# Kernel optimization log

Measured on AMD Instinct MI355X. Metric: run time of the kernel, lower is better.

Reference implementation:

```python
import jax, jax.numpy as jnp
import numpy as np

SQRT_2_OVER_PI = 0.7978845608028654

def gelu_tanh(x):
    return 0.5 * x * (1.0 + jnp.tanh(SQRT_2_OVER_PI * (x + 0.044715 * x ** 3)))

def setup_inputs() -> dict:
    key = jax.random.key(0)
    ks = jax.random.split(key, 16)
    B, L, H, Dk, Dv = 4, 512, 8, 64, 64
    dm = H * Dk
    inp = {
        'q': jax.random.normal(ks[0], (B, L, dm), jnp.float32),
        'k': jax.random.normal(ks[1], (B, L, dm), jnp.float32),
        'v': jax.random.normal(ks[2], (B, L, dm), jnp.float32),
        'vec_adj_k': jax.random.normal(ks[3], (B, L, L, Dk), jnp.float32),
        'vec_adj_v': jax.random.normal(ks[4], (B, L, L, Dv), jnp.float32),
        'adj_k': jax.random.randint(ks[5], (B, L, L), 0, 2, jnp.int32),
        'adj_v': jax.random.randint(ks[6], (B, L, L), 0, 2, jnp.int32),
        # learned params (Linear weights stored as [in, out]; y = x @ W)
        'w_qs': jax.random.normal(ks[7], (dm, H * Dk), jnp.float32) * 0.02,
        'w_ks': jax.random.normal(ks[8], (dm, H * Dk), jnp.float32) * 0.02,
        'w_vs': jax.random.normal(ks[9], (dm, H * Dv), jnp.float32) * 0.02,
        'w_fc': jax.random.normal(ks[10], (H * Dk, H * Dk), jnp.float32) * 0.02,
        'w_nw': jax.random.normal(ks[11], (H * Dk, 1), jnp.float32) * 0.02,
        'w_self': jax.random.normal(ks[12], (H * Dk, H * Dk), jnp.float32) * 0.02,
        'w_dd': jax.random.normal(ks[13], (H * Dk, H * Dk), jnp.float32) * 0.02,
    }
    return inp

def reference(q, k, v, vec_adj_k, vec_adj_v, adj_k, adj_v,
              w_qs, w_ks, w_vs, w_fc, w_nw, w_self, w_dd):
    H, Dk, Dv = 8, 64, 64
    B, L, dm = q.shape
    temperature = Dk ** 0.5
    residual = q
    # projections -> [B, H, L, D]
    qh = (q @ w_qs).reshape(B, L, H, Dk).transpose(0, 2, 1, 3)
    kh = (k @ w_ks).reshape(B, L, H, Dk).transpose(0, 2, 1, 3)
    vh = (v @ w_vs).reshape(B, L, H, Dv).transpose(0, 2, 1, 3)
    qs = qh / temperature
    # inner_(q, k, vec_adj_k, flag=True): content + relative-position scores
    scores = jnp.einsum('bhld,bhmd->bhlm', qs, kh) \
           + jnp.einsum('bhld,blmd->bhlm', qs, vec_adj_k)  # [B,H,L,L]
    # adjacency mask (mask == 0 -> -10000)
    scores = jnp.where(adj_k[:, None, :, :] == 0, jnp.float32(-10000.0), scores)
    attn = jax.nn.softmax(scores, axis=-1)
    # inner_(attn, v, vec_adj_v, flag=False)
    out = jnp.einsum('bhlm,bhmd->bhld', attn, vh) \
        + jnp.einsum('bhlm,blmd->bhld', attn, vec_adj_v)
    qc = out.transpose(0, 2, 1, 3).reshape(B, L, H * Dv)  # [B,L,dm]
    # masked neighbor aggregation (GNN stage)
    adj_f = adj_k.astype(qc.dtype)
    nn_num = adj_f.sum(-1)                                  # [B,L]
    denom = jnp.where(nn_num >= 1.0, nn_num, 1.0)
    node_weight = jax.nn.sigmoid((qc @ w_nw)[..., 0])       # [B,L]
    self_info = qc @ w_self
    dd_info = qc @ w_dd
    dd_weight = node_weight[:, None, :] * adj_f             # [B,L,L]
    agg = jnp.matmul(dd_weight, dd_info) / denom[..., None]
    qo = gelu_tanh((self_info + agg) @ w_fc)
    qo = residual + qo
    return (qo, attn)
```

## Files before the change

kernel.cpp:

```cpp
#include <hip/hip_runtime.h>
#include <cstdint>

#define NB 4
#define NL 512
#define NH 8
#define ND 64
#define NDM 512

typedef __attribute__((ext_vector_type(8))) short short8;
typedef __attribute__((ext_vector_type(4))) float f32x4;

__device__ __forceinline__ unsigned short f2bf(float f){
  union { float f; unsigned u; } v; v.f = f;
  unsigned r = (v.u + 0x7fffu + ((v.u >> 16) & 1u)) >> 16;
  return (unsigned short)r;
}

__device__ __forceinline__ short8 ld8(const unsigned short* p){
  return *(const short8*)p;
}

__device__ __forceinline__ f32x4 mfma16(short8 a, short8 b, f32x4 c){
  return __builtin_amdgcn_mfma_f32_16x16x32_bf16(a, b, c, 0, 0, 0);
}

__device__ __forceinline__ float gelu_tanh(float x){
  float u = 0.7978845608028654f * (x + 0.044715f * x * x * x);
  return 0.5f * x * (1.f + tanhf(u));
}

__global__ __launch_bounds__(256) void k_prep(const float* __restrict__ q,
    const float* __restrict__ k, const float* __restrict__ v,
    unsigned short* __restrict__ xin,
    const float* __restrict__ wqs, const float* __restrict__ wks,
    const float* __restrict__ wvs, const float* __restrict__ wself,
    const float* __restrict__ wdd, const float* __restrict__ wfc,
    unsigned short* __restrict__ Wt){
  int blk = blockIdx.x;
  int t = threadIdx.x;
  if (blk < 3072){
    int i = blk * 256 + t;
    int w = i >> 18, r = i & 262143;
    const float* src = (w == 0) ? q : (w == 1) ? k : v;
    float4 f = *(const float4*)(src + (size_t)r * 4);
    unsigned lo = (unsigned)f2bf(f.x) | ((unsigned)f2bf(f.y) << 16);
    unsigned hi = (unsigned)f2bf(f.z) | ((unsigned)f2bf(f.w) << 16);
    uint2 o; o.x = lo; o.y = hi;
    *(uint2*)(xin + (size_t)w * 1048576 + (size_t)r * 4) = o;
  } else {
    int i = (blk - 3072) * 256 + t;
    int w = i >> 13;
    int rr = i & 8191;
    int kg = rr >> 9;
    int n  = rr & 511;
    int k0 = kg * 32;
    const float* src = (w == 0) ? wqs : (w == 1) ? wks : (w == 2) ? wvs :
                       (w == 3) ? wself : (w == 4) ? wdd : wfc;
    unsigned pk[16];
#pragma unroll
    for (int j = 0; j < 16; j++){
      float a = src[(size_t)(k0 + 2 * j) * 512 + n];
      float b = src[(size_t)(k0 + 2 * j + 1) * 512 + n];
      pk[j] = (unsigned)f2bf(a) | ((unsigned)f2bf(b) << 16);
    }
    uint4* o4 = (uint4*)(Wt + (size_t)w * 262144 + (size_t)n * 512 + k0);
    o4[0] = make_uint4(pk[0],  pk[1],  pk[2],  pk[3]);
    o4[1] = make_uint4(pk[4],  pk[5],  pk[6],  pk[7]);
    o4[2] = make_uint4(pk[8],  pk[9],  pk[10], pk[11]);
    o4[3] = make_uint4(pk[12], pk[13], pk[14], pk[15]);
  }
}

__global__ __launch_bounds__(256) void k_proj(const unsigned short* __restrict__ xin,
    const unsigned short* __restrict__ Wt, unsigned short* __restrict__ qsb,
    unsigned short* __restrict__ khb, unsigned short* __restrict__ vhT){
  int wid0 = blockIdx.x * 4 + (threadIdx.x >> 6);
  int mode = wid0 >> 10;
  int wid = wid0 & 1023;
  int lane = threadIdx.x & 63;
  int tm = wid >> 5, tn = wid & 31;
  int r = lane & 15, q = lane >> 4;
  const unsigned short* X = xin + (size_t)mode * 1048576;
  const unsigned short* W = Wt + (size_t)mode * 262144;
  unsigned short* dst = (mode == 0) ? qsb : (mode == 1) ? khb : vhT;
  const unsigned short* A  = X + (size_t)(tm * 16 + r) * 512 + q * 8;
  const unsigned short* Bp = W + (size_t)(tn * 16 + r) * 512 + q * 8;
  f32x4 acc = {0.f, 0.f, 0.f, 0.f};
  for (int kk = 0; kk < 512; kk += 32) acc = mfma16(ld8(A + kk), ld8(Bp + kk), acc);
  int col = tn * 16 + r;
  int h = col >> 6, d = col & 63;
  float sc = (mode == 0) ? 0.125f : 1.0f;
  for (int i = 0; i < 4; i++){
    int row = tm * 16 + q * 4 + i;
    int b = row >> 9, l = row & 511;
    float vv = acc[i] * sc;
    size_t idx = (mode == 2) ? ((size_t)((b * 8 + h) * 64 + d) * 512 + l)
                             : ((size_t)((b * 8 + h) * 512 + l) * 64 + d);
    dst[idx] = f2bf(vv);
  }
}

__global__ __launch_bounds__(256) void k_scores(const unsigned short* __restrict__ qs,
    const unsigned short* __restrict__ kh, float* __restrict__ attnF){
  int wid = blockIdx.x * 4 + (threadIdx.x >> 6);
  int lane = threadIdx.x & 63;
  int bh = wid >> 8;
  int rest = wid & 255;
  int tm = rest >> 3, tg = rest & 7;
  int r = lane & 15, q = lane >> 4;
  const unsigned short* A = qs + (size_t)bh * 512 * 64 + (size_t)(tm * 16 + r) * 64 + q * 8;
  short8 a0 = ld8(A), a1 = ld8(A + 32);
  float* C = attnF + (size_t)bh * 512 * 512;
  for (int tn = tg * 4; tn < tg * 4 + 4; tn++){
    const unsigned short* Bp = kh + (size_t)bh * 512 * 64 + (size_t)(tn * 16 + r) * 64 + q * 8;
    f32x4 acc = {0.f, 0.f, 0.f, 0.f};
    acc = mfma16(a0, ld8(Bp),      acc);
    acc = mfma16(a1, ld8(Bp + 32), acc);
    for (int i = 0; i < 4; i++){
      int row = tm * 16 + q * 4 + i;
      C[(size_t)row * 512 + tn * 16 + r] = acc[i];
    }
  }
}

__global__ __launch_bounds__(256) void k_relsoft(const unsigned short* __restrict__ qs,
    const float* __restrict__ vak, const int* __restrict__ adj,
    float* __restrict__ attnF, unsigned short* __restrict__ attn_bf){
  int bid = blockIdx.x;
  int b = bid >> 9, l = bid & 511;
  int t = threadIdx.x, lane = t & 63, w = t >> 6;
  __shared__ __align__(16) unsigned short qsA[16 * 64];
  __shared__ __align__(16) unsigned short vkt[128 * 72];
  __shared__ float sc[8 * 512];
  __shared__ int adjs[512];
  for (int j = 0; j < 4; j++){
    int e = t + j * 256;
    int m = e >> 6, d = e & 63;
    qsA[e] = (m < 8) ? qs[((size_t)((b * 8 + m) * 512 + l)) * 64 + d] : (unsigned short)0;
  }
  for (int j = 0; j < 16; j++){
    int e = t + j * 256;
    int h = e >> 9, m = e & 511;
    sc[e] = attnF[((size_t)(b * 8 + h) * 512 + l) * 512 + m];
  }
  adjs[t]       = adj[(size_t)bid * 512 + t];
  adjs[t + 256] = adj[(size_t)bid * 512 + t + 256];
  __syncthreads();
  int r = lane & 15, q = lane >> 4;
  short8 a0 = ld8(qsA + r * 64 + q * 8);
  short8 a1 = ld8(qsA + r * 64 + 32 + q * 8);
  const float* vrow = vak + (size_t)bid * 512 * 64;
  for (int c = 0; c < 4; c++){
    for (int it = 0; it < 8; it++){
      int i4 = it * 256 + t;
      int m = i4 >> 4, d4 = (i4 & 15) * 4;
      const float4 f = *(const float4*)(vrow + (size_t)(c * 128 + m) * 64 + d4);
      unsigned p0 = (unsigned)f2bf(f.x) | ((unsigned)f2bf(f.y) << 16);
      unsigned p1 = (unsigned)f2bf(f.z) | ((unsigned)f2bf(f.w) << 16);
      uint2 pp; pp.x = p0; pp.y = p1;
      *(uint2*)(&vkt[m * 72 + d4]) = pp;
    }
    __syncthreads();
    for (int nt2 = 0; nt2 < 2; nt2++){
      int nt = w * 2 + nt2;
      const unsigned short* bp = vkt + (nt * 16 + r) * 72 + q * 8;
      f32x4 acc = {0.f, 0.f, 0.f, 0.f};
      acc = mfma16(a0, ld8(bp),      acc);
      acc = mfma16(a1, ld8(bp + 32), acc);
      if (q < 2){
        for (int i = 0; i < 4; i++){
          int h = q * 4 + i;
          sc[h * 512 + c * 128 + nt * 16 + r] += acc[i];
        }
      }
    }
    __syncthreads();
  }
  for (int hh = 0; hh < 2; hh++){
    int h = w * 2 + hh;
    float v[8]; float mx = -3.0e38f;
    for (int i = 0; i < 8; i++){
      int m = lane + i * 64;
      float s = sc[h * 512 + m];
      if (adjs[m] == 0) s = -10000.0f;
      v[i] = s; mx = fmaxf(mx, s);
    }
    for (int off = 32; off; off >>= 1) mx = fmaxf(mx, __shfl_xor(mx, off, 64));
    float sum = 0.f;
    for (int i = 0; i < 8; i++){ v[i] = __expf(v[i] - mx); sum += v[i]; }
    for (int off = 32; off; off >>= 1) sum += __shfl_xor(sum, off, 64);
    float inv = 1.f / sum;
    size_t base = ((size_t)(b * 8 + h) * 512 + l) * 512;
    for (int i = 0; i < 8; i++){
      int m = lane + i * 64;
      float p2 = v[i] * inv;
      attnF[base + m] = p2;
      attn_bf[base + m] = f2bf(p2);
    }
  }
}

__global__ __launch_bounds__(256) void k_outc(const unsigned short* __restrict__ attn_bf,
    const unsigned short* __restrict__ vhT, float* __restrict__ qc){
  int wid = blockIdx.x * 4 + (threadIdx.x >> 6);
  int lane = threadIdx.x & 63;
  int bh = wid >> 7, tile = wid & 127;
  int tm = tile >> 2, tn = tile & 3;
  int r = lane & 15, q = lane >> 4;
  const unsigned short* A  = attn_bf + (size_t)bh * 512 * 512 + (size_t)(tm * 16 + r) * 512 + q * 8;
  const unsigned short* Bp = vhT + (size_t)bh * 64 * 512 + (size_t)(tn * 16 + r) * 512 + q * 8;
  f32x4 acc = {0.f, 0.f, 0.f, 0.f};
  for (int k = 0; k < 512; k += 32) acc = mfma16(ld8(A + k), ld8(Bp + k), acc);
  int b = bh >> 3, h = bh & 7;
  int d = tn * 16 + r;
  for (int i = 0; i < 4; i++){
    int lrow = tm * 16 + q * 4 + i;
    qc[(size_t)(b * 512 + lrow) * 512 + h * 64 + d] = acc[i];
  }
}

__global__ __launch_bounds__(256) void k_outrel(const unsigned short* __restrict__ attn_bf,
    const float* __restrict__ vav, const float* __restrict__ qc,
    const int* __restrict__ adj, const float* __restrict__ wnw,
    unsigned short* __restrict__ qc_bf, float* __restrict__ nw, float* __restrict__ invden){
  int bid = blockIdx.x;
  int b = bid >> 9, l = bid & 511;
  int t = threadIdx.x, lane = t & 63, w = t >> 6;
  __shared__ __align__(16) unsigned short vvT[64 * 136];
  __shared__ float orL[512];
  __shared__ float redf[4];
  __shared__ int redi[4];
  int r = lane & 15, q = lane >> 4;
  int h8 = r & 7;
  const float* vrow = vav + (size_t)bid * 512 * 64;
  const unsigned short* arow = attn_bf + ((size_t)(b * 8 + h8) * 512 + l) * 512;
  f32x4 acc = {0.f, 0.f, 0.f, 0.f};
  for (int c = 0; c < 4; c++){
    for (int it = 0; it < 8; it++){
      int i4 = it * 256 + t;
      int m = i4 >> 4, d4 = (i4 & 15) * 4;
      const float4 f = *(const float4*)(vrow + (size_t)(c * 128 + m) * 64 + d4);
      vvT[(d4    ) * 136 + m] = f2bf(f.x);
      vvT[(d4 + 1) * 136 + m] = f2bf(f.y);
      vvT[(d4 + 2) * 136 + m] = f2bf(f.z);
      vvT[(d4 + 3) * 136 + m] = f2bf(f.w);
    }
    __syncthreads();
    for (int s = 0; s < 4; s++){
      int kk = c * 128 + s * 32;
      short8 av = ld8(arow + kk + q * 8);
      short8 bv = ld8(vvT + (w * 16 + r) * 136 + s * 32 + q * 8);
      acc = mfma16(av, bv, acc);
    }
    __syncthreads();
  }
  if (q < 2){
    for (int i = 0; i < 4; i++){
      int h = q * 4 + i;
      orL[h * 64 + w * 16 + r] = acc[i];
    }
  }
  __syncthreads();
  float part = 0.f; int asum = 0;
  for (int j = 0; j < 2; j++){
    int e = t + j * 256;
    float val = qc[(size_t)bid * 512 + e] + orL[e];
    qc_bf[(size_t)bid * 512 + e] = f2bf(val);
    part += val * wnw[e];
    asum += adj[(size_t)bid * 512 + e];
  }
  for (int off = 32; off; off >>= 1){
    part += __shfl_xor(part, off, 64);
    asum += __shfl_xor(asum, off, 64);
  }
  if (lane == 0){ redf[w] = part; redi[w] = asum; }
  __syncthreads();
  if (t == 0){
    float tot = redf[0] + redf[1] + redf[2] + redf[3];
    int at = redi[0] + redi[1] + redi[2] + redi[3];
    nw[bid] = 1.f / (1.f + __expf(-tot));
    invden[bid] = 1.f / ((at >= 1) ? (float)at : 1.f);
  }
}

__global__ __launch_bounds__(256) void k_post(const unsigned short* __restrict__ qcb,
    const unsigned short* __restrict__ Wself, const unsigned short* __restrict__ Wdd,
    float* __restrict__ selfi, unsigned short* __restrict__ ddT,
    const int* __restrict__ adj, const float* __restrict__ nw,
    const float* __restrict__ invden, unsigned short* __restrict__ ddw){
  __shared__ __align__(16) unsigned short ldsT[64 * 20];
  int blk = blockIdx.x;
  int t = threadIdx.x;
  if (blk < 2048){
    int mode = blk >> 10;
    int wv = t >> 6;
    int wid = (blk & 1023) * 4 + wv;
    int lane = t & 63;
    int tm = wid >> 5, tn = wid & 31;
    int r = lane & 15, q = lane >> 4;
    const unsigned short* W = mode ? Wdd : Wself;
    const unsigned short* A  = qcb + (size_t)(tm * 16 + r) * 512 + q * 8;
    const unsigned short* Bp = W + (size_t)(tn * 16 + r) * 512 + q * 8;
    f32x4 acc = {0.f, 0.f, 0.f, 0.f};
    for (int kk = 0; kk < 512; kk += 32) acc = mfma16(ld8(A + kk), ld8(Bp + kk), acc);
    int col = tn * 16 + r;
    if (mode == 0){
      for (int i = 0; i < 4; i++){
        int row = tm * 16 + q * 4 + i;
        selfi[(size_t)row * 512 + col] = acc[i];
      }
    } else {
      int nLocal = wv * 16 + r;
      for (int i = 0; i < 4; i++) ldsT[nLocal * 20 + q * 4 + i] = f2bf(acc[i]);
      __syncthreads();
      int tmB = ((blk & 1023) * 4) >> 5;
      int tnBase = ((blk & 1023) * 4) & 31;
      int n = t >> 2, part = t & 3;
      ushort4 val = *(const ushort4*)(&ldsT[n * 20 + part * 4]);
      int b = (tmB * 16) >> 9;
      int m0 = (tmB * 16) & 511;
      int nGlob = tnBase * 16 + n;
      *(ushort4*)(&ddT[((size_t)(b * 512 + nGlob)) * 512 + m0 + part * 4]) = val;
    }
  } else {
    int i = (blk - 2048) * 256 + t;
    int b = i >> 18, rest = i & 262143;
    int l = rest >> 9, m = rest & 511;
    int a = adj[i];
    float v = a ? nw[b * 512 + m] * invden[b * 512 + l] : 0.f;
    ddw[i] = f2bf(v);
  }
}

__global__ __launch_bounds__(256) void k_agg(const unsigned short* __restrict__ ddw,
    const unsigned short* __restrict__ ddT, const float* __restrict__ selfi,
    unsigned short* __restrict__ xbf){
  int wid = blockIdx.x * 4 + (threadIdx.x >> 6);
  int lane = threadIdx.x & 63;
  int b = wid >> 10, tile = wid & 1023;
  int tm = tile >> 5, tn = tile & 31;
  int r = lane & 15, q = lane >> 4;
  const unsigned short* A  = ddw + (size_t)b * 262144 + (size_t)(tm * 16 + r) * 512 + q * 8;
  const unsigned short* Bp = ddT + (size_t)b * 262144 + (size_t)(tn * 16 + r) * 512 + q * 8;
  f32x4 acc = {0.f, 0.f, 0.f, 0.f};
  for (int k = 0; k < 512; k += 32) acc = mfma16(ld8(A + k), ld8(Bp + k), acc);
  int col = tn * 16 + r;
  for (int i = 0; i < 4; i++){
    int row = b * 512 + tm * 16 + q * 4 + i;
    float x = acc[i] + selfi[(size_t)row * 512 + col];
    xbf[(size_t)row * 512 + col] = f2bf(x);
  }
}

__global__ __launch_bounds__(256) void k_fc(const unsigned short* __restrict__ xbf,
    const unsigned short* __restrict__ W, const float* __restrict__ qin,
    float* __restrict__ qo){
  int wid = blockIdx.x * 4 + (threadIdx.x >> 6);
  int lane = threadIdx.x & 63;
  int tm = wid >> 5, tn = wid & 31;
  int r = lane & 15, q = lane >> 4;
  const unsigned short* A  = xbf + (size_t)(tm * 16 + r) * 512 + q * 8;
  const unsigned short* Bp = W + (size_t)(tn * 16 + r) * 512 + q * 8;
  f32x4 acc = {0.f, 0.f, 0.f, 0.f};
  for (int k = 0; k < 512; k += 32) acc = mfma16(ld8(A + k), ld8(Bp + k), acc);
  int col = tn * 16 + r;
  for (int i = 0; i < 4; i++){
    int row = tm * 16 + q * 4 + i;
    qo[(size_t)row * 512 + col] = qin[(size_t)row * 512 + col] + gelu_tanh(acc[i]);
  }
}

extern "C" void kernel_launch(void* const* d_in, const int* in_sizes, int n_in,
                              void* d_out, int out_size, void* d_ws, size_t ws_size,
                              hipStream_t stream){
  const float* q    = (const float*)d_in[0];
  const float* k    = (const float*)d_in[1];
  const float* v    = (const float*)d_in[2];
  const float* vak  = (const float*)d_in[3];
  const float* vav  = (const float*)d_in[4];
  const int*   adjk = (const int*)d_in[5];
  const float* wqs  = (const float*)d_in[7];
  const float* wks  = (const float*)d_in[8];
  const float* wvs  = (const float*)d_in[9];
  const float* wfc  = (const float*)d_in[10];
  const float* wnw  = (const float*)d_in[11];
  const float* wself= (const float*)d_in[12];
  const float* wdd  = (const float*)d_in[13];

  float* qo    = (float*)d_out;
  float* attnF = qo + 1048576;

  char* p = (char*)d_ws;
  unsigned short* xin   = (unsigned short*)p; p += 6291456;
  unsigned short* Wt    = (unsigned short*)p; p += 3145728;
  unsigned short* qsb   = (unsigned short*)p; p += 2097152;
  unsigned short* khb   = (unsigned short*)p; p += 2097152;
  unsigned short* vhT   = (unsigned short*)p; p += 2097152;
  unsigned short* attnb = (unsigned short*)p; p += 16777216;
  float*          qc    = (float*)p;          p += 4194304;
  unsigned short* qcb   = (unsigned short*)p; p += 2097152;
  float*          nw    = (float*)p;          p += 8192;
  float*          invd  = (float*)p;          p += 8192;
  float*          selfi = (float*)p;          p += 4194304;
  unsigned short* ddT   = (unsigned short*)p; p += 2097152;
  unsigned short* ddw   = (unsigned short*)p; p += 2097152;
  unsigned short* xbf   = (unsigned short*)p; p += 2097152;

  k_prep<<<3264, 256, 0, stream>>>(q, k, v, xin, wqs, wks, wvs, wself, wdd, wfc, Wt);
  k_proj<<<3072, 256, 0, stream>>>(xin, Wt, qsb, khb, vhT);
  k_scores<<<2048, 256, 0, stream>>>(qsb, khb, attnF);
  k_relsoft<<<2048, 256, 0, stream>>>(qsb, vak, adjk, attnF, attnb);
  k_outc<<<1024, 256, 0, stream>>>(attnb, vhT, qc);
  k_outrel<<<2048, 256, 0, stream>>>(attnb, vav, qc, adjk, wnw, qcb, nw, invd);
  k_post<<<6144, 256, 0, stream>>>(qcb, Wt + 786432, Wt + 1048576, selfi, ddT,
                                   adjk, nw, invd, ddw);
  k_agg<<<1024, 256, 0, stream>>>(ddw, ddT, selfi, xbf);
  k_fc<<<1024, 256, 0, stream>>>(xbf, Wt + 1310720, q, qo);
}
```

Before: 713.7 us.

## Use 64x64 per-wave MFMA tiles and drop LDS staging in relative kernels

```diff
diff --git a/kernel.cpp b/kernel.cpp
--- a/kernel.cpp
+++ b/kernel.cpp
@@ -1,11 +1,6 @@
 #include <hip/hip_runtime.h>
 #include <cstdint>
 
-#define NB 4
-#define NL 512
-#define NH 8
-#define ND 64
-#define NDM 512
 
 typedef __attribute__((ext_vector_type(8))) short short8;
 typedef __attribute__((ext_vector_type(4))) float f32x4;
@@ -27,6 +22,36 @@
 __device__ __forceinline__ float gelu_tanh(float x){
   float u = 0.7978845608028654f * (x + 0.044715f * x * x * x);
   return 0.5f * x * (1.f + tanhf(u));
+}
+
+__device__ __forceinline__ short8 pack8(float4 f0, float4 f1){
+  short8 s;
+  s[0] = (short)f2bf(f0.x); s[1] = (short)f2bf(f0.y);
+  s[2] = (short)f2bf(f0.z); s[3] = (short)f2bf(f0.w);
+  s[4] = (short)f2bf(f1.x); s[5] = (short)f2bf(f1.y);
+  s[6] = (short)f2bf(f1.z); s[7] = (short)f2bf(f1.w);
+  return s;
+}
+
+template<int LDA, int LDB, int KSTEPS>
+__device__ __forceinline__ void gemm64(const unsigned short* __restrict__ A,
+                                       const unsigned short* __restrict__ Bp,
+                                       f32x4 acc[4][4]){
+#pragma unroll 2
+  for (int ks = 0; ks < KSTEPS; ks++){
+    int kk = ks * 32;
+    short8 a[4], b[4];
+#pragma unroll
+    for (int i = 0; i < 4; i++){
+      a[i] = ld8(A + (size_t)i * 16 * LDA + kk);
+      b[i] = ld8(Bp + (size_t)i * 16 * LDB + kk);
+    }
+#pragma unroll
+    for (int i = 0; i < 4; i++)
+#pragma unroll
+      for (int j = 0; j < 4; j++)
+        acc[i][j] = mfma16(a[i], b[j], acc[i][j]);
+  }
 }
 
 __global__ __launch_bounds__(256) void k_prep(const float* __restrict__ q,
@@ -74,53 +99,60 @@
 __global__ __launch_bounds__(256) void k_proj(const unsigned short* __restrict__ xin,
     const unsigned short* __restrict__ Wt, unsigned short* __restrict__ qsb,
     unsigned short* __restrict__ khb, unsigned short* __restrict__ vhT){
-  int wid0 = blockIdx.x * 4 + (threadIdx.x >> 6);
-  int mode = wid0 >> 10;
-  int wid = wid0 & 1023;
+  int wid = blockIdx.x * 4 + (threadIdx.x >> 6);
+  int mode = wid >> 8;
+  int tile = wid & 255;
+  int tm = tile >> 3, tn = tile & 7;
   int lane = threadIdx.x & 63;
-  int tm = wid >> 5, tn = wid & 31;
-  int r = lane & 15, q = lane >> 4;
+  int r = lane & 15, qq = lane >> 4;
   const unsigned short* X = xin + (size_t)mode * 1048576;
   const unsigned short* W = Wt + (size_t)mode * 262144;
   unsigned short* dst = (mode == 0) ? qsb : (mode == 1) ? khb : vhT;
-  const unsigned short* A  = X + (size_t)(tm * 16 + r) * 512 + q * 8;
-  const unsigned short* Bp = W + (size_t)(tn * 16 + r) * 512 + q * 8;
-  f32x4 acc = {0.f, 0.f, 0.f, 0.f};
-  for (int kk = 0; kk < 512; kk += 32) acc = mfma16(ld8(A + kk), ld8(Bp + kk), acc);
-  int col = tn * 16 + r;
-  int h = col >> 6, d = col & 63;
-  float sc = (mode == 0) ? 0.125f : 1.0f;
-  for (int i = 0; i < 4; i++){
-    int row = tm * 16 + q * 4 + i;
-    int b = row >> 9, l = row & 511;
-    float vv = acc[i] * sc;
-    size_t idx = (mode == 2) ? ((size_t)((b * 8 + h) * 64 + d) * 512 + l)
-                             : ((size_t)((b * 8 + h) * 512 + l) * 64 + d);
-    dst[idx] = f2bf(vv);
-  }
+  const unsigned short* A  = X + (size_t)(tm * 64 + r) * 512 + qq * 8;
+  const unsigned short* Bp = W + (size_t)(tn * 64 + r) * 512 + qq * 8;
+  f32x4 acc[4][4] = {};
+  gemm64<512, 512, 16>(A, Bp, acc);
+  float scv = (mode == 0) ? 0.125f : 1.0f;
+  int h = tn;
+#pragma unroll
+  for (int i = 0; i < 4; i++)
+#pragma unroll
+    for (int j = 0; j < 4; j++)
+#pragma unroll
+      for (int e = 0; e < 4; e++){
+        int row = tm * 64 + i * 16 + qq * 4 + e;
+        int d = j * 16 + r;
+        int bb = row >> 9, l = row & 511;
+        unsigned short val = f2bf(acc[i][j][e] * scv);
+        size_t idx = (mode == 2) ? ((size_t)((bb * 8 + h) * 64 + d) * 512 + l)
+                                 : ((size_t)((bb * 8 + h) * 512 + l) * 64 + d);
+        dst[idx] = val;
+      }
 }
 
 __global__ __launch_bounds__(256) void k_scores(const unsigned short* __restrict__ qs,
     const unsigned short* __restrict__ kh, float* __restrict__ attnF){
   int wid = blockIdx.x * 4 + (threadIdx.x >> 6);
+  int bh = wid >> 6;
+  int tile = wid & 63;
+  int tm = tile >> 3, tn = tile & 7;
   int lane = threadIdx.x & 63;
-  int bh = wid >> 8;
-  int rest = wid & 255;
-  int tm = rest >> 3, tg = rest & 7;
-  int r = lane & 15, q = lane >> 4;
-  const unsigned short* A = qs + (size_t)bh * 512 * 64 + (size_t)(tm * 16 + r) * 64 + q * 8;
-  short8 a0 = ld8(A), a1 = ld8(A + 32);
-  float* C = attnF + (size_t)bh * 512 * 512;
-  for (int tn = tg * 4; tn < tg * 4 + 4; tn++){
-    const unsigned short* Bp = kh + (size_t)bh * 512 * 64 + (size_t)(tn * 16 + r) * 64 + q * 8;
-    f32x4 acc = {0.f, 0.f, 0.f, 0.f};
-    acc = mfma16(a0, ld8(Bp),      acc);
-    acc = mfma16(a1, ld8(Bp + 32), acc);
-    for (int i = 0; i < 4; i++){
-      int row = tm * 16 + q * 4 + i;
-      C[(size_t)row * 512 + tn * 16 + r] = acc[i];
-    }
-  }
+  int r = lane & 15, qq = lane >> 4;
+  const unsigned short* A  = qs + (size_t)bh * 32768 + (size_t)(tm * 64 + r) * 64 + qq * 8;
+  const unsigned short* Bp = kh + (size_t)bh * 32768 + (size_t)(tn * 64 + r) * 64 + qq * 8;
+  f32x4 acc[4][4] = {};
+  gemm64<64, 64, 2>(A, Bp, acc);
+  float* C = attnF + (size_t)bh * 262144;
+#pragma unroll
+  for (int i = 0; i < 4; i++)
+#pragma unroll
+    for (int j = 0; j < 4; j++)
+#pragma unroll
+      for (int e = 0; e < 4; e++){
+        int row = tm * 64 + i * 16 + qq * 4 + e;
+        int col = tn * 64 + j * 16 + r;
+        C[(size_t)row * 512 + col] = acc[i][j][e];
+      }
 }
 
 __global__ __launch_bounds__(256) void k_relsoft(const unsigned short* __restrict__ qs,
@@ -130,7 +162,6 @@
   int b = bid >> 9, l = bid & 511;
   int t = threadIdx.x, lane = t & 63, w = t >> 6;
   __shared__ __align__(16) unsigned short qsA[16 * 64];
-  __shared__ __align__(16) unsigned short vkt[128 * 72];
   __shared__ float sc[8 * 512];
   __shared__ int adjs[512];
   for (int j = 0; j < 4; j++){
@@ -146,36 +177,34 @@
   adjs[t]       = adj[(size_t)bid * 512 + t];
   adjs[t + 256] = adj[(size_t)bid * 512 + t + 256];
   __syncthreads();
-  int r = lane & 15, q = lane >> 4;
-  short8 a0 = ld8(qsA + r * 64 + q * 8);
-  short8 a1 = ld8(qsA + r * 64 + 32 + q * 8);
-  const float* vrow = vak + (size_t)bid * 512 * 64;
+  int r = lane & 15, qq = lane >> 4;
+  short8 a0 = ld8(qsA + r * 64 + qq * 8);
+  short8 a1 = ld8(qsA + r * 64 + 32 + qq * 8);
+  const float* vrow = vak + (size_t)bid * 32768;
+#pragma unroll
   for (int c = 0; c < 4; c++){
-    for (int it = 0; it < 8; it++){
-      int i4 = it * 256 + t;
-      int m = i4 >> 4, d4 = (i4 & 15) * 4;
-      const float4 f = *(const float4*)(vrow + (size_t)(c * 128 + m) * 64 + d4);
-      unsigned p0 = (unsigned)f2bf(f.x) | ((unsigned)f2bf(f.y) << 16);
-      unsigned p1 = (unsigned)f2bf(f.z) | ((unsigned)f2bf(f.w) << 16);
-      uint2 pp; pp.x = p0; pp.y = p1;
-      *(uint2*)(&vkt[m * 72 + d4]) = pp;
-    }
-    __syncthreads();
+#pragma unroll
     for (int nt2 = 0; nt2 < 2; nt2++){
       int nt = w * 2 + nt2;
-      const unsigned short* bp = vkt + (nt * 16 + r) * 72 + q * 8;
+      int m0 = c * 128 + nt * 16 + r;
+      const float* p = vrow + (size_t)m0 * 64 + qq * 8;
+      float4 f0 = *(const float4*)(p);
+      float4 f1 = *(const float4*)(p + 4);
+      float4 f2 = *(const float4*)(p + 32);
+      float4 f3 = *(const float4*)(p + 36);
       f32x4 acc = {0.f, 0.f, 0.f, 0.f};
-      acc = mfma16(a0, ld8(bp),      acc);
-      acc = mfma16(a1, ld8(bp + 32), acc);
-      if (q < 2){
+      acc = mfma16(a0, pack8(f0, f1), acc);
+      acc = mfma16(a1, pack8(f2, f3), acc);
+      if (qq < 2){
+#pragma unroll
         for (int i = 0; i < 4; i++){
-          int h = q * 4 + i;
+          int h = qq * 4 + i;
           sc[h * 512 + c * 128 + nt * 16 + r] += acc[i];
         }
       }
     }
-    __syncthreads();
-  }
+  }
+  __syncthreads();
   for (int hh = 0; hh < 2; hh++){
     int h = w * 2 + hh;
     float v[8]; float mx = -3.0e38f;
@@ -203,20 +232,25 @@
 __global__ __launch_bounds__(256) void k_outc(const unsigned short* __restrict__ attn_bf,
     const unsigned short* __restrict__ vhT, float* __restrict__ qc){
   int wid = blockIdx.x * 4 + (threadIdx.x >> 6);
+  int bh = wid >> 3;
+  int tm = wid & 7;
   int lane = threadIdx.x & 63;
-  int bh = wid >> 7, tile = wid & 127;
-  int tm = tile >> 2, tn = tile & 3;
-  int r = lane & 15, q = lane >> 4;
-  const unsigned short* A  = attn_bf + (size_t)bh * 512 * 512 + (size_t)(tm * 16 + r) * 512 + q * 8;
-  const unsigned short* Bp = vhT + (size_t)bh * 64 * 512 + (size_t)(tn * 16 + r) * 512 + q * 8;
-  f32x4 acc = {0.f, 0.f, 0.f, 0.f};
-  for (int k = 0; k < 512; k += 32) acc = mfma16(ld8(A + k), ld8(Bp + k), acc);
+  int r = lane & 15, qq = lane >> 4;
+  const unsigned short* A  = attn_bf + (size_t)bh * 262144 + (size_t)(tm * 64 + r) * 512 + qq * 8;
+  const unsigned short* Bp = vhT + (size_t)bh * 32768 + (size_t)r * 512 + qq * 8;
+  f32x4 acc[4][4] = {};
+  gemm64<512, 512, 16>(A, Bp, acc);
   int b = bh >> 3, h = bh & 7;
-  int d = tn * 16 + r;
-  for (int i = 0; i < 4; i++){
-    int lrow = tm * 16 + q * 4 + i;
-    qc[(size_t)(b * 512 + lrow) * 512 + h * 64 + d] = acc[i];
-  }
+#pragma unroll
+  for (int i = 0; i < 4; i++)
+#pragma unroll
+    for (int j = 0; j < 4; j++)
+#pragma unroll
+      for (int e = 0; e < 4; e++){
+        int lrow = tm * 64 + i * 16 + qq * 4 + e;
+        int d = j * 16 + r;
+        qc[(size_t)(b * 512 + lrow) * 512 + h * 64 + d] = acc[i][j][e];
+      }
 }
 
 __global__ __launch_bounds__(256) void k_outrel(const unsigned short* __restrict__ attn_bf,
@@ -226,38 +260,36 @@
   int bid = blockIdx.x;
   int b = bid >> 9, l = bid & 511;
   int t = threadIdx.x, lane = t & 63, w = t >> 6;
-  __shared__ __align__(16) unsigned short vvT[64 * 136];
   __shared__ float orL[512];
   __shared__ float redf[4];
   __shared__ int redi[4];
-  int r = lane & 15, q = lane >> 4;
+  int r = lane & 15, qq = lane >> 4;
   int h8 = r & 7;
-  const float* vrow = vav + (size_t)bid * 512 * 64;
+  const float* vrow = vav + (size_t)bid * 32768;
   const unsigned short* arow = attn_bf + ((size_t)(b * 8 + h8) * 512 + l) * 512;
   f32x4 acc = {0.f, 0.f, 0.f, 0.f};
+  int dcol = w * 16 + r;
+#pragma unroll
   for (int c = 0; c < 4; c++){
-    for (int it = 0; it < 8; it++){
-      int i4 = it * 256 + t;
-      int m = i4 >> 4, d4 = (i4 & 15) * 4;
-      const float4 f = *(const float4*)(vrow + (size_t)(c * 128 + m) * 64 + d4);
-      vvT[(d4    ) * 136 + m] = f2bf(f.x);
-      vvT[(d4 + 1) * 136 + m] = f2bf(f.y);
-      vvT[(d4 + 2) * 136 + m] = f2bf(f.z);
-      vvT[(d4 + 3) * 136 + m] = f2bf(f.w);
-    }
-    __syncthreads();
+#pragma unroll
     for (int s = 0; s < 4; s++){
       int kk = c * 128 + s * 32;
-      short8 av = ld8(arow + kk + q * 8);
-      short8 bv = ld8(vvT + (w * 16 + r) * 136 + s * 32 + q * 8);
+      short8 av = ld8(arow + kk + qq * 8);
+      float fv[8];
+#pragma unroll
+      for (int j = 0; j < 8; j++)
+        fv[j] = vrow[(size_t)(kk + qq * 8 + j) * 64 + dcol];
+      short8 bv;
+#pragma unroll
+      for (int j = 0; j < 8; j++) bv[j] = (short)f2bf(fv[j]);
       acc = mfma16(av, bv, acc);
     }
-    __syncthreads();
-  }
-  if (q < 2){
+  }
+  if (qq < 2){
+#pragma unroll
     for (int i = 0; i < 4; i++){
-      int h = q * 4 + i;
-      orL[h * 64 + w * 16 + r] = acc[i];
+      int h = qq * 4 + i;
+      orL[h * 64 + dcol] = acc[i];
     }
   }
   __syncthreads();
@@ -288,47 +320,52 @@
     float* __restrict__ selfi, unsigned short* __restrict__ ddT,
     const int* __restrict__ adj, const float* __restrict__ nw,
     const float* __restrict__ invden, unsigned short* __restrict__ ddw){
-  __shared__ __align__(16) unsigned short ldsT[64 * 20];
   int blk = blockIdx.x;
   int t = threadIdx.x;
-  if (blk < 2048){
-    int mode = blk >> 10;
-    int wv = t >> 6;
-    int wid = (blk & 1023) * 4 + wv;
+  if (blk < 128){
+    int mode = blk >> 6;
+    int wid = (blk & 63) * 4 + (t >> 6);
+    int tm = wid >> 3, tn = wid & 7;
     int lane = t & 63;
-    int tm = wid >> 5, tn = wid & 31;
-    int r = lane & 15, q = lane >> 4;
+    int r = lane & 15, qq = lane >> 4;
     const unsigned short* W = mode ? Wdd : Wself;
-    const unsigned short* A  = qcb + (size_t)(tm * 16 + r) * 512 + q * 8;
-    const unsigned short* Bp = W + (size_t)(tn * 16 + r) * 512 + q * 8;
-    f32x4 acc = {0.f, 0.f, 0.f, 0.f};
-    for (int kk = 0; kk < 512; kk += 32) acc = mfma16(ld8(A + kk), ld8(Bp + kk), acc);
-    int col = tn * 16 + r;
-    if (mode == 0){
-      for (int i = 0; i < 4; i++){
-        int row = tm * 16 + q * 4 + i;
-        selfi[(size_t)row * 512 + col] = acc[i];
-      }
-    } else {
-      int nLocal = wv * 16 + r;
-      for (int i = 0; i < 4; i++) ldsT[nLocal * 20 + q * 4 + i] = f2bf(acc[i]);
-      __syncthreads();
-      int tmB = ((blk & 1023) * 4) >> 5;
-      int tnBase = ((blk & 1023) * 4) & 31;
-      int n = t >> 2, part = t & 3;
-      ushort4 val = *(const ushort4*)(&ldsT[n * 20 + part * 4]);
-      int b = (tmB * 16) >> 9;
-      int m0 = (tmB * 16) & 511;
-      int nGlob = tnBase * 16 + n;
-      *(ushort4*)(&ddT[((size_t)(b * 512 + nGlob)) * 512 + m0 + part * 4]) = val;
-    }
+    const unsigned short* A  = qcb + (size_t)(tm * 64 + r) * 512 + qq * 8;
+    const unsigned short* Bp = W + (size_t)(tn * 64 + r) * 512 + qq * 8;
+    f32x4 acc[4][4] = {};
+    gemm64<512, 512, 16>(A, Bp, acc);
+#pragma unroll
+    for (int i = 0; i < 4; i++)
+#pragma unroll
+      for (int j = 0; j < 4; j++)
+#pragma unroll
+        for (int e = 0; e < 4; e++){
+          int row = tm * 64 + i * 16 + qq * 4 + e;
+          int col = tn * 64 + j * 16 + r;
+          if (mode == 0)
+            selfi[(size_t)row * 512 + col] = acc[i][j][e];
+          else {
+            int bb = row >> 9, m = row & 511;
+            ddT[((size_t)(bb * 512 + col)) * 512 + m] = f2bf(acc[i][j][e]);
+          }
+        }
   } else {
-    int i = (blk - 2048) * 256 + t;
-    int b = i >> 18, rest = i & 262143;
-    int l = rest >> 9, m = rest & 511;
-    int a = adj[i];
-    float v = a ? nw[b * 512 + m] * invden[b * 512 + l] : 0.f;
-    ddw[i] = f2bf(v);
+    int i8 = ((blk - 128) * 256 + t) * 8;
+    int bb = i8 >> 18, rest = i8 & 262143;
+    int l = rest >> 9, m0 = rest & 511;
+    int4 a0 = *(const int4*)(adj + i8);
+    int4 a1 = *(const int4*)(adj + i8 + 4);
+    float id = invden[bb * 512 + l];
+    const float* nwb = nw + bb * 512 + m0;
+    short8 o;
+    o[0] = a0.x ? (short)f2bf(nwb[0] * id) : (short)0;
+    o[1] = a0.y ? (short)f2bf(nwb[1] * id) : (short)0;
+    o[2] = a0.z ? (short)f2bf(nwb[2] * id) : (short)0;
+    o[3] = a0.w ? (short)f2bf(nwb[3] * id) : (short)0;
+    o[4] = a1.x ? (short)f2bf(nwb[4] * id) : (short)0;
+    o[5] = a1.y ? (short)f2bf(nwb[5] * id) : (short)0;
+    o[6] = a1.z ? (short)f2bf(nwb[6] * id) : (short)0;
+    o[7] = a1.w ? (short)f2bf(nwb[7] * id) : (short)0;
+    *(short8*)(ddw + i8) = o;
   }
 }
 
@@ -336,38 +373,49 @@
     const unsigned short* __restrict__ ddT, const float* __restrict__ selfi,
     unsigned short* __restrict__ xbf){
   int wid = blockIdx.x * 4 + (threadIdx.x >> 6);
+  int b = wid >> 6;
+  int tile = wid & 63;
+  int tm = tile >> 3, tn = tile & 7;
   int lane = threadIdx.x & 63;
-  int b = wid >> 10, tile = wid & 1023;
-  int tm = tile >> 5, tn = tile & 31;
-  int r = lane & 15, q = lane >> 4;
-  const unsigned short* A  = ddw + (size_t)b * 262144 + (size_t)(tm * 16 + r) * 512 + q * 8;
-  const unsigned short* Bp = ddT + (size_t)b * 262144 + (size_t)(tn * 16 + r) * 512 + q * 8;
-  f32x4 acc = {0.f, 0.f, 0.f, 0.f};
-  for (int k = 0; k < 512; k += 32) acc = mfma16(ld8(A + k), ld8(Bp + k), acc);
-  int col = tn * 16 + r;
-  for (int i = 0; i < 4; i++){
-    int row = b * 512 + tm * 16 + q * 4 + i;
-    float x = acc[i] + selfi[(size_t)row * 512 + col];
-    xbf[(size_t)row * 512 + col] = f2bf(x);
-  }
+  int r = lane & 15, qq = lane >> 4;
+  const unsigned short* A  = ddw + (size_t)b * 262144 + (size_t)(tm * 64 + r) * 512 + qq * 8;
+  const unsigned short* Bp = ddT + (size_t)b * 262144 + (size_t)(tn * 64 + r) * 512 + qq * 8;
+  f32x4 acc[4][4] = {};
+  gemm64<512, 512, 16>(A, Bp, acc);
+#pragma unroll
+  for (int i = 0; i < 4; i++)
+#pragma unroll
+    for (int j = 0; j < 4; j++)
+#pragma unroll
+      for (int e = 0; e < 4; e++){
+        int row = b * 512 + tm * 64 + i * 16 + qq * 4 + e;
+        int col = tn * 64 + j * 16 + r;
+        float x = acc[i][j][e] + selfi[(size_t)row * 512 + col];
+        xbf[(size_t)row * 512 + col] = f2bf(x);
+      }
 }
 
 __global__ __launch_bounds__(256) void k_fc(const unsigned short* __restrict__ xbf,
     const unsigned short* __restrict__ W, const float* __restrict__ qin,
     float* __restrict__ qo){
   int wid = blockIdx.x * 4 + (threadIdx.x >> 6);
+  int tm = wid >> 3, tn = wid & 7;
   int lane = threadIdx.x & 63;
-  int tm = wid >> 5, tn = wid & 31;
-  int r = lane & 15, q = lane >> 4;
-  const unsigned short* A  = xbf + (size_t)(tm * 16 + r) * 512 + q * 8;
-  const unsigned short* Bp = W + (size_t)(tn * 16 + r) * 512 + q * 8;
-  f32x4 acc = {0.f, 0.f, 0.f, 0.f};
-  for (int k = 0; k < 512; k += 32) acc = mfma16(ld8(A + k), ld8(Bp + k), acc);
-  int col = tn * 16 + r;
-  for (int i = 0; i < 4; i++){
-    int row = tm * 16 + q * 4 + i;
-    qo[(size_t)row * 512 + col] = qin[(size_t)row * 512 + col] + gelu_tanh(acc[i]);
-  }
+  int r = lane & 15, qq = lane >> 4;
+  const unsigned short* A  = xbf + (size_t)(tm * 64 + r) * 512 + qq * 8;
+  const unsigned short* Bp = W + (size_t)(tn * 64 + r) * 512 + qq * 8;
+  f32x4 acc[4][4] = {};
+  gemm64<512, 512, 16>(A, Bp, acc);
+#pragma unroll
+  for (int i = 0; i < 4; i++)
+#pragma unroll
+    for (int j = 0; j < 4; j++)
+#pragma unroll
+      for (int e = 0; e < 4; e++){
+        int row = tm * 64 + i * 16 + qq * 4 + e;
+        int col = tn * 64 + j * 16 + r;
+        qo[(size_t)row * 512 + col] = qin[(size_t)row * 512 + col] + gelu_tanh(acc[i][j][e]);
+      }
 }
 
 extern "C" void kernel_launch(void* const* d_in, const int* in_sizes, int n_in,
@@ -407,13 +455,13 @@
   unsigned short* xbf   = (unsigned short*)p; p += 2097152;
 
   k_prep<<<3264, 256, 0, stream>>>(q, k, v, xin, wqs, wks, wvs, wself, wdd, wfc, Wt);
-  k_proj<<<3072, 256, 0, stream>>>(xin, Wt, qsb, khb, vhT);
-  k_scores<<<2048, 256, 0, stream>>>(qsb, khb, attnF);
+  k_proj<<<192, 256, 0, stream>>>(xin, Wt, qsb, khb, vhT);
+  k_scores<<<512, 256, 0, stream>>>(qsb, khb, attnF);
   k_relsoft<<<2048, 256, 0, stream>>>(qsb, vak, adjk, attnF, attnb);
-  k_outc<<<1024, 256, 0, stream>>>(attnb, vhT, qc);
+  k_outc<<<64, 256, 0, stream>>>(attnb, vhT, qc);
   k_outrel<<<2048, 256, 0, stream>>>(attnb, vav, qc, adjk, wnw, qcb, nw, invd);
-  k_post<<<6144, 256, 0, stream>>>(qcb, Wt + 786432, Wt + 1048576, selfi, ddT,
-                                   adjk, nw, invd, ddw);
-  k_agg<<<1024, 256, 0, stream>>>(ddw, ddT, selfi, xbf);
-  k_fc<<<1024, 256, 0, stream>>>(xbf, Wt + 1310720, q, qo);
-}
+  k_post<<<640, 256, 0, stream>>>(qcb, Wt + 786432, Wt + 1048576, selfi, ddT,
+                                  adjk, nw, invd, ddw);
+  k_agg<<<64, 256, 0, stream>>>(ddw, ddT, selfi, xbf);
+  k_fc<<<64, 256, 0, stream>>>(xbf, Wt + 1310720, q, qo);
+}
```

After: 708.6 us. About the same (-0.7%).
